# Kernel tuning notes

Measured on AMD Instinct MI355X. Metric: run time of the kernel, lower is better.

Reference implementation:

```python
import jax, jax.numpy as jnp
import numpy as np

EMB = 512
HEADS = 8
B, T = 4, 1024


def setup_inputs() -> dict:
    key = jax.random.key(0)
    k1, k2, k3, k4, k5 = jax.random.split(key, 5)
    scale = 1.0 / np.sqrt(EMB)
    x = jax.random.normal(k1, (B, T, EMB), dtype=jnp.float32)
    # Linear(emb, emb*heads, bias=False) weights, stored as [in, out] for x @ W
    Wk = jax.random.normal(k2, (EMB, EMB * HEADS), dtype=jnp.float32) * scale
    Wq = jax.random.normal(k3, (EMB, EMB * HEADS), dtype=jnp.float32) * scale
    Wv = jax.random.normal(k4, (EMB, EMB * HEADS), dtype=jnp.float32) * scale
    Wu = jax.random.normal(k5, (EMB * HEADS, EMB), dtype=jnp.float32) * (1.0 / np.sqrt(EMB * HEADS))
    return {"x": x, "Wk": Wk, "Wq": Wq, "Wv": Wv, "Wu": Wu}


def reference(x, Wk, Wq, Wv, Wu):
    b, t, k = x.shape
    h = HEADS
    # projections -> [b, h, t, k]
    keys = (x @ Wk).reshape(b, t, h, k).transpose(0, 2, 1, 3)
    queries = (x @ Wq).reshape(b, t, h, k).transpose(0, 2, 1, 3)
    values = (x @ Wv).reshape(b, t, h, k).transpose(0, 2, 1, 3)
    # NOTE: original computes bmm(keys, queries^T): dot[i,j] = key_i . query_j
    dot = jnp.einsum('bhik,bhjk->bhij', keys, queries)  # [b,h,t,t]
    # mask_fn: only upper-triangle (offset=1) entries that are EXACTLY zero get -inf
    triu = jnp.triu(jnp.ones((t, t), dtype=bool), k=1)
    final_mask = triu & (dot == 0)
    dot = jnp.where(final_mask, -jnp.inf, dot)
    attn = jax.nn.softmax(dot, axis=-1)
    out = jnp.einsum('bhij,bhjk->bhik', attn, values)  # [b,h,t,k]
    out = out.transpose(0, 2, 1, 3).reshape(b, t, h * k)
    return out @ Wu
```

## Files before the change

kernel.cpp:

```cpp
#include <hip/hip_runtime.h>
#include <stdint.h>

typedef _Float16 f16x8 __attribute__((ext_vector_type(8)));
typedef float f32x4 __attribute__((ext_vector_type(4)));

__device__ __forceinline__ unsigned short f2h(float f) {
  _Float16 h = (_Float16)f;
  return __builtin_bit_cast(unsigned short, h);
}

#if __has_builtin(__builtin_amdgcn_global_load_lds)
#define HAVE_GLL 1
__device__ __forceinline__ void gload_lds16(const void* g, void* l) {
  auto gp = reinterpret_cast<const __attribute__((address_space(1))) void*>(
      reinterpret_cast<uintptr_t>(g));
  auto lp = reinterpret_cast<__attribute__((address_space(3))) void*>(
      reinterpret_cast<uintptr_t>(l));
  __builtin_amdgcn_global_load_lds(gp, lp, 16, 0, 0);
}
#else
#define HAVE_GLL 0
#endif

__device__ __forceinline__ void transpose_core(const float* in, unsigned short* out,
                                               int R, int C, int c0, int r0) {
  __shared__ float t[32][33];
  int tx = threadIdx.x & 31, ty = threadIdx.x >> 5;
#pragma unroll
  for (int i = 0; i < 32; i += 8)
    t[ty + i][tx] = in[(long)(r0 + ty + i) * C + (c0 + tx)];
  __syncthreads();
#pragma unroll
  for (int i = 0; i < 32; i += 8)
    out[(long)(c0 + ty + i) * R + (r0 + tx)] = f2h(t[tx][ty + i]);
}

__global__ __launch_bounds__(256) void k_setup(
    const float* __restrict__ x, const float* __restrict__ Wq, const float* __restrict__ Wk,
    const float* __restrict__ Wv, const float* __restrict__ Wu,
    unsigned short* __restrict__ Xh, unsigned short* __restrict__ Wqt,
    unsigned short* __restrict__ Wkt, unsigned short* __restrict__ Wvh,
    unsigned short* __restrict__ Wut) {
  int z = blockIdx.z;
  if (z == 0) {
    transpose_core(Wq, Wqt, 512, 4096, blockIdx.x * 32, blockIdx.y * 32);
  } else if (z == 1) {
    transpose_core(Wk, Wkt, 512, 4096, blockIdx.x * 32, blockIdx.y * 32);
  } else if (z == 2) {
    transpose_core(Wu, Wut, 4096, 512, blockIdx.y * 32, blockIdx.x * 32);
  } else {
    const float* in = (z == 3) ? x : Wv;
    unsigned short* out = (z == 3) ? Xh : Wvh;
    int i = (blockIdx.y * 128 + blockIdx.x) * 256 + threadIdx.x;
    float4 v = reinterpret_cast<const float4*>(in)[i];
    ushort4 o;
    o.x = f2h(v.x); o.y = f2h(v.y); o.z = f2h(v.z); o.w = f2h(v.w);
    reinterpret_cast<ushort4*>(out)[i] = o;
  }
}

template <int OUT, int BVU>
__device__ __forceinline__ void gemm_core(unsigned short* __restrict__ As,
                                          unsigned short* __restrict__ Bs,
                                          const unsigned short* __restrict__ A,
                                          const unsigned short* __restrict__ B,
                                          void* __restrict__ Cv, int K, int lda, int ldb,
                                          int ldc, long coff, int m0, int n0, int kbase) {
  int tid = threadIdx.x;
  int wid = tid >> 6, lane = tid & 63;
  int wm = (wid >> 1) * 64, wn = (wid & 1) * 64;
  int rq = lane >> 4, rl = lane & 15;

  f32x4 acc[4][4];
#pragma unroll
  for (int i = 0; i < 4; ++i)
#pragma unroll
    for (int j = 0; j < 4; ++j) acc[i][j] = (f32x4){0.f, 0.f, 0.f, 0.f};

#if HAVE_GLL
  int cg = (lane & 7) ^ ((lane >> 3) & 7);
  int rl8 = lane >> 3;
#endif

  for (int k0 = 0; k0 < K; k0 += 64) {
    long bko;
    if (BVU) {
      int kk = kbase + k0;
      bko = (long)(kk >> 10) * 2097152 + (kk & 1023);
    } else {
      bko = k0;
    }
    __syncthreads();
#if HAVE_GLL
#pragma unroll
    for (int t = 0; t < 4; ++t) {
      int r = wid * 32 + t * 8;
      gload_lds16(&A[(long)(m0 + r + rl8) * lda + k0 + cg * 8], &As[r * 64]);
      gload_lds16(&B[(long)(n0 + r + rl8) * ldb + bko + cg * 8], &Bs[r * 64]);
    }
#else
#pragma unroll
    for (int it = 0; it < 4; ++it) {
      int idx = tid + it * 256;
      int r = idx >> 3, c = idx & 7;
      int cs = c ^ (r & 7);
      *reinterpret_cast<uint4*>(&As[r * 64 + cs * 8]) =
          *reinterpret_cast<const uint4*>(&A[(long)(m0 + r) * lda + k0 + c * 8]);
      *reinterpret_cast<uint4*>(&Bs[r * 64 + cs * 8]) =
          *reinterpret_cast<const uint4*>(&B[(long)(n0 + r) * ldb + bko + c * 8]);
    }
#endif
    __syncthreads();
#pragma unroll
    for (int ks = 0; ks < 2; ++ks) {
      f16x8 af[4], bfr[4];
      int kc = ks * 4 + rq;
#pragma unroll
      for (int i = 0; i < 4; ++i) {
        int ra = wm + i * 16 + rl;
        af[i] = *reinterpret_cast<const f16x8*>(&As[ra * 64 + ((kc ^ (ra & 7)) << 3)]);
        int rb = wn + i * 16 + rl;
        bfr[i] = *reinterpret_cast<const f16x8*>(&Bs[rb * 64 + ((kc ^ (rb & 7)) << 3)]);
      }
#pragma unroll
      for (int i = 0; i < 4; ++i)
#pragma unroll
        for (int j = 0; j < 4; ++j)
          acc[i][j] = __builtin_amdgcn_mfma_f32_16x16x32_f16(af[i], bfr[j], acc[i][j], 0, 0, 0);
    }
  }

#pragma unroll
  for (int i = 0; i < 4; ++i)
#pragma unroll
    for (int j = 0; j < 4; ++j)
#pragma unroll
      for (int r = 0; r < 4; ++r) {
        int row = m0 + wm + i * 16 + rq * 4 + r;
        int col = n0 + wn + j * 16 + rl;
        float v = acc[i][j][r];
        if (OUT == 1)
          reinterpret_cast<unsigned short*>(Cv)[coff + (long)row * ldc + col] = f2h(v);
        else
          atomicAdd(&reinterpret_cast<float*>(Cv)[coff + (long)row * ldc + col], v);
      }
}

#define DECL_LDS \
  __shared__ unsigned short As[128 * 64]; \
  __shared__ unsigned short Bs[128 * 64];

__global__ __launch_bounds__(256, 2) void k_gemm_qkw(
    const unsigned short* __restrict__ X, const unsigned short* __restrict__ Wqt,
    const unsigned short* __restrict__ Wkt, const unsigned short* __restrict__ Wvh,
    const unsigned short* __restrict__ Wut, unsigned short* __restrict__ Qb,
    unsigned short* __restrict__ Kb, unsigned short* __restrict__ Wvut) {
  DECL_LDS
  int c = blockIdx.x, w = blockIdx.y;
  const unsigned short *A, *B;
  unsigned short* C;
  int lda, ldb, ldc, m0, n0;
  long coff;
  if (w < 256) {
    int z = w >> 7, r = w & 127;
    int x = 4 * c + (r & 3), y = r >> 2;
    A = X; B = (z == 0) ? Wqt : Wkt; C = (z == 0) ? Qb : Kb;
    lda = 512; ldb = 512; ldc = 4096; coff = 0; m0 = y * 128; n0 = x * 128;
  } else {
    int wp = w - 256;
    A = Wut + c * 512; B = Wvh + c * 512; C = Wvut + (long)c * 262144;
    lda = 4096; ldb = 4096; ldc = 512; coff = 0;
    m0 = ((wp >> 2) & 3) * 128; n0 = (wp & 3) * 128;
  }
  gemm_core<1, 0>(As, Bs, A, B, C, 512, lda, ldb, ldc, coff, m0, n0, 0);
}

__global__ __launch_bounds__(256, 2) void k_gemm_sv(
    const unsigned short* __restrict__ X, const unsigned short* __restrict__ Qb,
    const unsigned short* __restrict__ Kb, const unsigned short* __restrict__ Wvut,
    unsigned short* __restrict__ Pb, unsigned short* __restrict__ VUt) {
  DECL_LDS
  int c = blockIdx.x, w = blockIdx.y;
  const unsigned short *A, *B;
  unsigned short* C;
  int lda, ldb, ldc, m0, n0;
  long coff;
  if (w < 256) {
    int z = c + 8 * (w >> 6), t = w & 63;
    int b = z >> 3, h = z & 7;
    long off = (long)b * 4194304 + h * 512;
    A = Kb + off; B = Qb + off; C = Pb;
    lda = 4096; ldb = 4096; ldc = 8192;
    coff = (long)b * 8388608 + h * 1024;
    m0 = (t >> 3) * 128; n0 = (t & 7) * 128;
  } else {
    int wp = w - 256;
    A = Wvut; B = X; C = VUt;
    lda = 512; ldb = 512; ldc = 4096; coff = 0;
    m0 = (4 * c + (wp & 3)) * 128; n0 = (wp >> 2) * 128;
  }
  gemm_core<1, 0>(As, Bs, A, B, C, 512, lda, ldb, ldc, coff, m0, n0, 0);
}

__global__ __launch_bounds__(256, 2) void k_gemm_out(
    const unsigned short* __restrict__ Pb, const unsigned short* __restrict__ VUt,
    float* __restrict__ out) {
  DECL_LDS
  int c = blockIdx.x, w = blockIdx.y;
  int g = c + 8 * (w >> 4);
  int r = w & 15;
  int b = g >> 3, kc = (g >> 1) & 3, ih = g & 1;
  int y = ih * 4 + (r >> 2);
  int x = r & 3;
  gemm_core<2, 1>(As, Bs, Pb + (long)b * 8388608 + kc * 2048, VUt + (long)b * 1024,
                  out, 2048, 8192, 4096, 512, (long)b * 524288, y * 128, x * 128,
                  kc * 2048);
}

__global__ __launch_bounds__(256) void k_softmax_x(unsigned short* __restrict__ S) {
  int g = blockIdx.y * 4 + (threadIdx.x >> 6);
  int b = g >> 10, i = g & 1023;
  long base = (long)b * 8388608 + (long)i * 8192 + (long)blockIdx.x * 1024;
  int lane = threadIdx.x & 63;
  f16x8* p = reinterpret_cast<f16x8*>(S + base);
  f16x8 a = p[lane * 2], bb = p[lane * 2 + 1];
  float v[16];
#pragma unroll
  for (int q = 0; q < 8; ++q) { v[q] = (float)a[q]; v[8 + q] = (float)bb[q]; }
  float m = v[0];
#pragma unroll
  for (int q = 1; q < 16; ++q) m = fmaxf(m, v[q]);
#pragma unroll
  for (int o = 32; o; o >>= 1) m = fmaxf(m, __shfl_xor(m, o));
  float s = 0.f;
#pragma unroll
  for (int q = 0; q < 16; ++q) { v[q] = __expf(v[q] - m); s += v[q]; }
#pragma unroll
  for (int o = 32; o; o >>= 1) s += __shfl_xor(s, o);
  float inv = 1.0f / s;
  f16x8 oa, ob;
#pragma unroll
  for (int q = 0; q < 8; ++q) {
    oa[q] = (_Float16)(v[q] * inv);
    ob[q] = (_Float16)(v[8 + q] * inv);
  }
  p[lane * 2] = oa;
  p[lane * 2 + 1] = ob;
}

__global__ void k_sentinel(float* out, float v) { out[0] = v; }

extern "C" void kernel_launch(void* const* d_in, const int* in_sizes, int n_in,
                              void* d_out, int out_size, void* d_ws, size_t ws_size,
                              hipStream_t stream) {
  const float* x  = (const float*)d_in[0];
  const float* Wk = (const float*)d_in[1];
  const float* Wq = (const float*)d_in[2];
  const float* Wv = (const float*)d_in[3];
  const float* Wu = (const float*)d_in[4];
  float* out = (float*)d_out;

  const long SZ_X = 4096L * 512;
  const long SZ_W = 512L * 4096;
  const size_t NEED = 188743680;

  if (ws_size < NEED) {
    hipMemsetAsync(d_out, 0, (size_t)out_size * 4, stream);
    k_sentinel<<<1, 1, 0, stream>>>(out, (float)ws_size);
    return;
  }

  char* p = (char*)d_ws;
  unsigned short* Xbf  = (unsigned short*)p; p += SZ_X * 2;
  unsigned short* Wqt  = (unsigned short*)p; p += SZ_W * 2;
  unsigned short* Wkt  = (unsigned short*)p; p += SZ_W * 2;
  unsigned short* Wut  = (unsigned short*)p; p += SZ_W * 2;
  unsigned short* Wvut = (unsigned short*)p; p += SZ_W * 2;
  unsigned short* Qb   = (unsigned short*)p; p += 4096L * 4096 * 2;
  unsigned short* Kb   = (unsigned short*)p; p += 4096L * 4096 * 2;
  unsigned short* Pb   = (unsigned short*)p; p += 4096L * 8192 * 2;
  unsigned short* VUt  = (unsigned short*)p;
  unsigned short* Wvh  = VUt;

  hipMemsetAsync(d_out, 0, (size_t)out_size * 4, stream);

  k_setup<<<dim3(128, 16, 5), 256, 0, stream>>>(x, Wq, Wk, Wv, Wu, Xbf, Wqt, Wkt, Wvh, Wut);

  k_gemm_qkw<<<dim3(8, 272), 256, 0, stream>>>(Xbf, Wqt, Wkt, Wvh, Wut, Qb, Kb, Wvut);

  k_gemm_sv<<<dim3(8, 384), 256, 0, stream>>>(Xbf, Qb, Kb, Wvut, Pb, VUt);

  k_softmax_x<<<dim3(8, 1024), 256, 0, stream>>>(Pb);

  k_gemm_out<<<dim3(8, 64), 256, 0, stream>>>(Pb, VUt, out);
}
```

Baseline: 283.4 us.

## Reassociate QK^T via per-head Wk·Wq^T product to skip Q projection

Replaces the separate Q and K projections with a per-head 512x512 matrix G = Wk_h·Wq_h^T, then computes T = X·G and scores S = T·X^T. This removes one large 4096x4096x512 projection GEMM and the Q/K transposes, replacing them with small weight-only GEMMs. Output zeroing is folded into the setup kernel instead of a separate memset. The reassociation changes fp16 rounding order, which may shift numerics slightly.

```diff
diff --git a/kernel.cpp b/kernel.cpp
--- a/kernel.cpp
+++ b/kernel.cpp
@@ -38,24 +38,23 @@
 __global__ __launch_bounds__(256) void k_setup(
     const float* __restrict__ x, const float* __restrict__ Wq, const float* __restrict__ Wk,
     const float* __restrict__ Wv, const float* __restrict__ Wu,
-    unsigned short* __restrict__ Xh, unsigned short* __restrict__ Wqt,
-    unsigned short* __restrict__ Wkt, unsigned short* __restrict__ Wvh,
-    unsigned short* __restrict__ Wut) {
+    unsigned short* __restrict__ Xh, unsigned short* __restrict__ Wqf,
+    unsigned short* __restrict__ Wkf, unsigned short* __restrict__ Wvh,
+    unsigned short* __restrict__ Wut, float* __restrict__ out) {
   int z = blockIdx.z;
-  if (z == 0) {
-    transpose_core(Wq, Wqt, 512, 4096, blockIdx.x * 32, blockIdx.y * 32);
-  } else if (z == 1) {
-    transpose_core(Wk, Wkt, 512, 4096, blockIdx.x * 32, blockIdx.y * 32);
-  } else if (z == 2) {
+  if (z == 2) {
     transpose_core(Wu, Wut, 4096, 512, blockIdx.y * 32, blockIdx.x * 32);
+  } else if (z == 5) {
+    int i = (blockIdx.y * 128 + blockIdx.x) * 256 + threadIdx.x;
+    reinterpret_cast<float4*>(out)[i] = (float4){0.f, 0.f, 0.f, 0.f};
   } else {
-    const float* in = (z == 3) ? x : Wv;
-    unsigned short* out = (z == 3) ? Xh : Wvh;
+    const float* in = (z == 0) ? Wq : (z == 1) ? Wk : (z == 3) ? x : Wv;
+    unsigned short* o = (z == 0) ? Wqf : (z == 1) ? Wkf : (z == 3) ? Xh : Wvh;
     int i = (blockIdx.y * 128 + blockIdx.x) * 256 + threadIdx.x;
     float4 v = reinterpret_cast<const float4*>(in)[i];
-    ushort4 o;
-    o.x = f2h(v.x); o.y = f2h(v.y); o.z = f2h(v.z); o.w = f2h(v.w);
-    reinterpret_cast<ushort4*>(out)[i] = o;
+    ushort4 u;
+    u.x = f2h(v.x); u.y = f2h(v.y); u.z = f2h(v.z); u.w = f2h(v.w);
+    reinterpret_cast<ushort4*>(o)[i] = u;
   }
 }
 
@@ -150,56 +149,51 @@
   __shared__ unsigned short As[128 * 64]; \
   __shared__ unsigned short Bs[128 * 64];
 
-__global__ __launch_bounds__(256, 2) void k_gemm_qkw(
-    const unsigned short* __restrict__ X, const unsigned short* __restrict__ Wqt,
-    const unsigned short* __restrict__ Wkt, const unsigned short* __restrict__ Wvh,
-    const unsigned short* __restrict__ Wut, unsigned short* __restrict__ Qb,
-    unsigned short* __restrict__ Kb, unsigned short* __restrict__ Wvut) {
+__global__ __launch_bounds__(256, 2) void k_gemm_w(
+    const unsigned short* __restrict__ Wqf, const unsigned short* __restrict__ Wkf,
+    const unsigned short* __restrict__ Wut, const unsigned short* __restrict__ Wvh,
+    unsigned short* __restrict__ Gt, unsigned short* __restrict__ Wvut) {
   DECL_LDS
   int c = blockIdx.x, w = blockIdx.y;
   const unsigned short *A, *B;
   unsigned short* C;
-  int lda, ldb, ldc, m0, n0;
-  long coff;
-  if (w < 256) {
-    int z = w >> 7, r = w & 127;
-    int x = 4 * c + (r & 3), y = r >> 2;
-    A = X; B = (z == 0) ? Wqt : Wkt; C = (z == 0) ? Qb : Kb;
-    lda = 512; ldb = 512; ldc = 4096; coff = 0; m0 = y * 128; n0 = x * 128;
-  } else {
-    int wp = w - 256;
-    A = Wut + c * 512; B = Wvh + c * 512; C = Wvut + (long)c * 262144;
-    lda = 4096; ldb = 4096; ldc = 512; coff = 0;
-    m0 = ((wp >> 2) & 3) * 128; n0 = (wp & 3) * 128;
-  }
-  gemm_core<1, 0>(As, Bs, A, B, C, 512, lda, ldb, ldc, coff, m0, n0, 0);
-}
-
-__global__ __launch_bounds__(256, 2) void k_gemm_sv(
-    const unsigned short* __restrict__ X, const unsigned short* __restrict__ Qb,
-    const unsigned short* __restrict__ Kb, const unsigned short* __restrict__ Wvut,
-    unsigned short* __restrict__ Pb, unsigned short* __restrict__ VUt) {
+  int t;
+  if (w < 16) { A = Wqf + c * 512; B = Wkf + c * 512; C = Gt + (long)c * 262144; t = w; }
+  else        { A = Wut + c * 512; B = Wvh + c * 512; C = Wvut + (long)c * 262144; t = w - 16; }
+  gemm_core<1, 0>(As, Bs, A, B, C, 512, 4096, 4096, 512, 0, (t >> 2) * 128, (t & 3) * 128, 0);
+}
+
+__global__ __launch_bounds__(256, 2) void k_gemm_tv(
+    const unsigned short* __restrict__ X, const unsigned short* __restrict__ Gt,
+    const unsigned short* __restrict__ Wvut, unsigned short* __restrict__ T,
+    unsigned short* __restrict__ VUt) {
   DECL_LDS
   int c = blockIdx.x, w = blockIdx.y;
   const unsigned short *A, *B;
   unsigned short* C;
-  int lda, ldb, ldc, m0, n0;
   long coff;
-  if (w < 256) {
-    int z = c + 8 * (w >> 6), t = w & 63;
-    int b = z >> 3, h = z & 7;
-    long off = (long)b * 4194304 + h * 512;
-    A = Kb + off; B = Qb + off; C = Pb;
-    lda = 4096; ldb = 4096; ldc = 8192;
-    coff = (long)b * 8388608 + h * 1024;
-    m0 = (t >> 3) * 128; n0 = (t & 7) * 128;
+  int m0, n0;
+  if (w < 128) {
+    A = X; B = Gt + (long)c * 262144; C = T;
+    coff = (long)c * 512; m0 = (w >> 2) * 128; n0 = (w & 3) * 128;
   } else {
-    int wp = w - 256;
+    int wp = w - 128;
     A = Wvut; B = X; C = VUt;
-    lda = 512; ldb = 512; ldc = 4096; coff = 0;
-    m0 = (4 * c + (wp & 3)) * 128; n0 = (wp >> 2) * 128;
-  }
-  gemm_core<1, 0>(As, Bs, A, B, C, 512, lda, ldb, ldc, coff, m0, n0, 0);
+    coff = 0; m0 = (4 * c + (wp & 3)) * 128; n0 = (wp >> 2) * 128;
+  }
+  gemm_core<1, 0>(As, Bs, A, B, C, 512, 512, 512, 4096, coff, m0, n0, 0);
+}
+
+__global__ __launch_bounds__(256, 2) void k_gemm_s(
+    const unsigned short* __restrict__ X, const unsigned short* __restrict__ T,
+    unsigned short* __restrict__ Pb) {
+  DECL_LDS
+  int c = blockIdx.x, w = blockIdx.y;
+  int z = c + 8 * (w >> 6), t = w & 63;
+  int b = z >> 3, h = z & 7;
+  gemm_core<1, 0>(As, Bs, T + (long)b * 4194304 + h * 512, X + (long)b * 524288, Pb,
+                  512, 4096, 512, 8192, (long)b * 8388608 + h * 1024,
+                  (t >> 3) * 128, (t & 7) * 128, 0);
 }
 
 __global__ __launch_bounds__(256, 2) void k_gemm_out(
@@ -272,23 +266,24 @@
 
   char* p = (char*)d_ws;
   unsigned short* Xbf  = (unsigned short*)p; p += SZ_X * 2;
-  unsigned short* Wqt  = (unsigned short*)p; p += SZ_W * 2;
-  unsigned short* Wkt  = (unsigned short*)p; p += SZ_W * 2;
+  unsigned short* Wqf  = (unsigned short*)p; p += SZ_W * 2;
+  unsigned short* Wkf  = (unsigned short*)p; p += SZ_W * 2;
   unsigned short* Wut  = (unsigned short*)p; p += SZ_W * 2;
   unsigned short* Wvut = (unsigned short*)p; p += SZ_W * 2;
-  unsigned short* Qb   = (unsigned short*)p; p += 4096L * 4096 * 2;
-  unsigned short* Kb   = (unsigned short*)p; p += 4096L * 4096 * 2;
+  unsigned short* Gt   = (unsigned short*)p; p += 8L * 512 * 512 * 2;
+  unsigned short* T    = (unsigned short*)p; p += 4096L * 4096 * 2;
   unsigned short* Pb   = (unsigned short*)p; p += 4096L * 8192 * 2;
   unsigned short* VUt  = (unsigned short*)p;
   unsigned short* Wvh  = VUt;
 
-  hipMemsetAsync(d_out, 0, (size_t)out_size * 4, stream);
-
-  k_setup<<<dim3(128, 16, 5), 256, 0, stream>>>(x, Wq, Wk, Wv, Wu, Xbf, Wqt, Wkt, Wvh, Wut);
-
-  k_gemm_qkw<<<dim3(8, 272), 256, 0, stream>>>(Xbf, Wqt, Wkt, Wvh, Wut, Qb, Kb, Wvut);
-
-  k_gemm_sv<<<dim3(8, 384), 256, 0, stream>>>(Xbf, Qb, Kb, Wvut, Pb, VUt);
+  k_setup<<<dim3(128, 16, 6), 256, 0, stream>>>(x, Wq, Wk, Wv, Wu, Xbf, Wqf, Wkf, Wvh,
+                                                Wut, out);
+
+  k_gemm_w<<<dim3(8, 32), 256, 0, stream>>>(Wqf, Wkf, Wut, Wvh, Gt, Wvut);
+
+  k_gemm_tv<<<dim3(8, 256), 256, 0, stream>>>(Xbf, Gt, Wvut, T, VUt);
+
+  k_gemm_s<<<dim3(8, 256), 256, 0, stream>>>(Xbf, T, Pb);
 
   k_softmax_x<<<dim3(8, 1024), 256, 0, stream>>>(Pb);
 
```

Result: faster. 263.2 us (-7.1%).
